# Kernel tuning notes

Hardware: AMD Instinct MI355X
Metric: run time of the kernel (lower is better)

## Reference

```python
import jax, jax.numpy as jnp
import numpy as np


def _hungarian(a):
    """Jonker-Volgenant / Kuhn-Munkres shortest-augmenting-path LAP solver.
    a: (n, n) float numpy cost matrix. Returns col_ind (int64, len n) such that
    row i is matched to column col_ind[i] (row_ind is implicitly arange(n),
    exactly like scipy.optimize.linear_sum_assignment on a square matrix).
    """
    n = a.shape[0]
    INF = np.inf
    u = np.zeros(n + 1)
    v = np.zeros(n + 1)
    p = np.zeros(n + 1, dtype=np.int64)   # p[j] = row currently matched to column j
    way = np.zeros(n + 1, dtype=np.int64)
    for i in range(1, n + 1):
        p[0] = i
        j0 = 0
        minv = np.full(n + 1, INF)
        used = np.zeros(n + 1, dtype=bool)
        while True:
            used[j0] = True
            i0 = p[j0]
            cur = a[i0 - 1] - u[i0] - v[1:]          # reduced costs of row i0
            free = ~used[1:]
            better = free & (cur < minv[1:])
            minv[1:] = np.where(better, cur, minv[1:])
            way[1:] = np.where(better, j0, way[1:])
            cand = np.where(free, minv[1:], INF)
            j1 = int(np.argmin(cand)) + 1
            delta = cand[j1 - 1]
            u[p[used]] += delta
            v[used] -= delta
            minv[1:] = np.where(free, minv[1:] - delta, minv[1:])
            j0 = j1
            if p[j0] == 0:
                break
        while j0 != 0:                               # augment along alternating path
            j1 = int(way[j0])
            p[j0] = p[j1]
            j0 = j1
    col_ind = np.zeros(n, dtype=np.int64)
    col_ind[p[1:] - 1] = np.arange(n)
    return col_ind


def _matching(input, target):
    sx = jnp.sum(input * input, axis=-1)
    sy = jnp.sum(target * target, axis=-1)
    cost = sx[:, :, None] + sy[:, None, :] - 2.0 * jnp.einsum('bkd,bmd->bkm', input, target)
    cost_np = np.asarray(jax.device_get(cost), dtype=np.float64)
    perms = np.stack([_hungarian(c) for c in cost_np])  # (B, k)
    return jnp.asarray(perms)


def setup_inputs() -> dict:
    key = jax.random.key(0)
    k1, k2 = jax.random.split(key)
    B, K, D = 512, 128, 512
    return {
        "input": jax.random.normal(k1, (B, K, D), dtype=jnp.float32),
        "target": jax.random.normal(k2, (B, K, D), dtype=jnp.float32),
    }


def reference(input, target):
    # Hungarian assignment is computed on detached costs (constant wrt grads).
    perms = _matching(input, target)                       # (B, k)
    matched_target = jnp.take_along_axis(target, perms[:, :, None], axis=1)
    # Per-batch mean over (k, d), then mean over batch == global mean (equal sizes).
    return jnp.mean((input - matched_target) ** 2)
```

## Files before the change

### kernel.cpp

```cpp
#include <hip/hip_runtime.h>
#include <hip/hip_bf16.h>

#define K_PTS 128
#define DIM   512
#define BK    32
#define XS_STRIDE 132

__device__ __forceinline__ int rdlane_i(int v, int lane) {
    return __builtin_amdgcn_readlane(v, lane);
}
__device__ __forceinline__ float rdlane_f(float v, int lane) {
    return __int_as_float(__builtin_amdgcn_readlane(__float_as_int(v), lane));
}
__device__ __forceinline__ void wave_fence() {
    asm volatile("s_waitcnt lgkmcnt(0)" ::: "memory");
}

#define DPP_ID 0xFFFFFFFFu

template <int CTRL, int RM>
__device__ __forceinline__ unsigned dpp_min1(unsigned k) {
    unsigned o = (unsigned)__builtin_amdgcn_update_dpp((int)DPP_ID, (int)k, CTRL, RM, 0xF, false);
    return min(k, o);
}
__device__ __forceinline__ unsigned wave_min_u32(unsigned k) {
    k = dpp_min1<0x111, 0xF>(k);
    k = dpp_min1<0x112, 0xF>(k);
    k = dpp_min1<0x114, 0xF>(k);
    k = dpp_min1<0x118, 0xF>(k);
    k = dpp_min1<0x142, 0xA>(k);
    k = dpp_min1<0x143, 0xC>(k);
    return (unsigned)rdlane_i((int)k, 63);
}
template <int CTRL, int RM>
__device__ __forceinline__ void dpp_min2(unsigned& best, unsigned& sec) {
    unsigned ob = (unsigned)__builtin_amdgcn_update_dpp((int)DPP_ID, (int)best, CTRL, RM, 0xF, false);
    unsigned os = (unsigned)__builtin_amdgcn_update_dpp((int)DPP_ID, (int)sec,  CTRL, RM, 0xF, false);
    sec  = min(max(best, ob), min(sec, os));
    best = min(best, ob);
}
__device__ __forceinline__ void wave_min2_u32(unsigned& best, unsigned& sec) {
    dpp_min2<0x111, 0xF>(best, sec);
    dpp_min2<0x112, 0xF>(best, sec);
    dpp_min2<0x114, 0xF>(best, sec);
    dpp_min2<0x118, 0xF>(best, sec);
    dpp_min2<0x142, 0xA>(best, sec);
    dpp_min2<0x143, 0xC>(best, sec);
    best = (unsigned)rdlane_i((int)best, 63);
    sec  = (unsigned)rdlane_i((int)sec, 63);
}

__global__ __launch_bounds__(256, 2)
void hungarian_mse_kernel(const float* __restrict__ X, const float* __restrict__ Y,
                          float* __restrict__ out, float inv_total) {
    const int b = blockIdx.x;
    const int t = threadIdx.x;

    __shared__ float A[K_PTS * K_PTS];
    __shared__ float sx_sh[K_PTS];
    __shared__ float sy_sh[K_PTS];
    __shared__ float u_sh[K_PTS];
    __shared__ int   rmatch[K_PTS];
    __shared__ int   wl[512];
    __shared__ int   wl_n;

    float* Xs = A;
    float* Ys = A + BK * XS_STRIDE;

    const float* Xg = X + (size_t)b * K_PTS * DIM;
    const float* Yg = Y + (size_t)b * K_PTS * DIM;

    float acc[8][8];
#pragma unroll
    for (int i = 0; i < 8; ++i)
#pragma unroll
        for (int j = 0; j < 8; ++j) acc[i][j] = 0.0f;

    float nrm = 0.0f;
    const int tx = t & 15;
    const int ty = t >> 4;

    for (int k0 = 0; k0 < DIM; k0 += BK) {
        __syncthreads();
#pragma unroll
        for (int i = 0; i < 4; ++i) {
            int idx = t + i * 256;
            int r  = idx >> 3;
            int kq = idx & 7;
            float4 vx = *(const float4*)(Xg + r * DIM + k0 + kq * 4);
            float4 vy = *(const float4*)(Yg + r * DIM + k0 + kq * 4);
            int kb = kq * 4;
            Xs[(kb + 0) * XS_STRIDE + r] = vx.x;
            Xs[(kb + 1) * XS_STRIDE + r] = vx.y;
            Xs[(kb + 2) * XS_STRIDE + r] = vx.z;
            Xs[(kb + 3) * XS_STRIDE + r] = vx.w;
            Ys[(kb + 0) * XS_STRIDE + r] = vy.x;
            Ys[(kb + 1) * XS_STRIDE + r] = vy.y;
            Ys[(kb + 2) * XS_STRIDE + r] = vy.z;
            Ys[(kb + 3) * XS_STRIDE + r] = vy.w;
        }
        __syncthreads();
        for (int kk = 0; kk < BK; ++kk) {
            const float* xrow = Xs + kk * XS_STRIDE;
            const float* yrow = Ys + kk * XS_STRIDE;
            float4 xa = *(const float4*)(xrow + ty * 8);
            float4 xb = *(const float4*)(xrow + ty * 8 + 4);
            float4 ya = *(const float4*)(yrow + tx * 8);
            float4 yb = *(const float4*)(yrow + tx * 8 + 4);
            float av[8] = {xa.x, xa.y, xa.z, xa.w, xb.x, xb.y, xb.z, xb.w};
            float bv[8] = {ya.x, ya.y, ya.z, ya.w, yb.x, yb.y, yb.z, yb.w};
#pragma unroll
            for (int i = 0; i < 8; ++i)
#pragma unroll
                for (int j = 0; j < 8; ++j)
                    acc[i][j] = fmaf(av[i], bv[j], acc[i][j]);
        }
        if (t < 128) {
#pragma unroll
            for (int kk = 0; kk < BK; ++kk) {
                float v = Xs[kk * XS_STRIDE + t];
                nrm = fmaf(v, v, nrm);
            }
        } else {
#pragma unroll
            for (int kk = 0; kk < BK; ++kk) {
                float v = Ys[kk * XS_STRIDE + (t - 128)];
                nrm = fmaf(v, v, nrm);
            }
        }
    }
    if (t < 128) sx_sh[t] = nrm; else sy_sh[t - 128] = nrm;
    if (t < 128) u_sh[t] = 0.0f;
    __syncthreads();
#pragma unroll
    for (int i = 0; i < 8; ++i) {
        int r = ty * 8 + i;
        float sxr = sx_sh[r];
        float4 o0, o1;
        o0.x = sxr + sy_sh[tx * 8 + 0] - 2.0f * acc[i][0];
        o0.y = sxr + sy_sh[tx * 8 + 1] - 2.0f * acc[i][1];
        o0.z = sxr + sy_sh[tx * 8 + 2] - 2.0f * acc[i][2];
        o0.w = sxr + sy_sh[tx * 8 + 3] - 2.0f * acc[i][3];
        o1.x = sxr + sy_sh[tx * 8 + 4] - 2.0f * acc[i][4];
        o1.y = sxr + sy_sh[tx * 8 + 5] - 2.0f * acc[i][5];
        o1.z = sxr + sy_sh[tx * 8 + 6] - 2.0f * acc[i][6];
        o1.w = sxr + sy_sh[tx * 8 + 7] - 2.0f * acc[i][7];
        *(float4*)&A[r * K_PTS + tx * 8]     = o0;
        *(float4*)&A[r * K_PTS + tx * 8 + 4] = o1;
    }
    __syncthreads();

    if (t < 64) {
        asm volatile("s_setprio 3");
        const int c0 = 2 * t, c1 = 2 * t + 1;
        float v0, v1;
        int p_lo = -1, p_hi = -1;

        rmatch[t] = -1; rmatch[t + 64] = -1;
        wave_fence();
        {
            float m0 = 1e30f, m1 = 1e30f;
            int a0 = 0, a1 = 0;
#pragma unroll 4
            for (int i = 0; i < K_PTS; ++i) {
                float2 cc = *(const float2*)&A[i * K_PTS + c0];
                if (cc.x < m0) { m0 = cc.x; a0 = i; }
                if (cc.y < m1) { m1 = cc.y; a1 = i; }
            }
            v0 = m0; v1 = m1;
            int w0 = atomicCAS(&rmatch[a0], -1, c0);
            if (w0 == -1) p_lo = a0;
            int w1 = atomicCAS(&rmatch[a1], -1, c1);
            if (w1 == -1) p_hi = a1;
        }
        wave_fence();

        *(float2*)&sy_sh[c0] = make_float2(v0, v1);
        wave_fence();
#pragma unroll
        for (int which = 0; which < 2; ++which) {
            int i  = t + which * 64;
            int j1 = rmatch[i];
            float mu = 1e30f;
            if (j1 >= 0) {
#pragma unroll 4
                for (int s = 0; s < 64; ++s) {
                    int jj = (s + t) & 63;
                    float2 cc = *(const float2*)&A[i * K_PTS + 2 * jj];
                    float2 vv = *(const float2*)&sy_sh[2 * jj];
                    float r0 = cc.x - vv.x;
                    float r1 = cc.y - vv.y;
                    if (2 * jj     != j1) mu = fminf(mu, r0);
                    if (2 * jj + 1 != j1) mu = fminf(mu, r1);
                }
            }
            sx_sh[i] = mu;
        }
        wave_fence();
        if (p_lo >= 0) { float mu = sx_sh[p_lo]; v0 = A[p_lo * K_PTS + c0] - mu; u_sh[p_lo] = mu; }
        if (p_hi >= 0) { float mu = sx_sh[p_hi]; v1 = A[p_hi * K_PTS + c1] - mu; u_sh[p_hi] = mu; }
        wave_fence();

        if (t == 0) {
            int n = 0;
            for (int i = 0; i < K_PTS; ++i) if (rmatch[i] < 0) wl[n++] = i;
            wl_n = n;
        }
        wave_fence();

        {
            int head = 0, tail = wl_n, steps = 0;
            int ni = -1;
            float2 nx = make_float2(0.0f, 0.0f);
            if (head < tail) {
                ni = wl[head];
                nx = *(const float2*)&A[ni * K_PTS + c0];
            }
            while (ni >= 0 && steps < 320) {
                ++steps;
                int i = ni;
                float2 cc = nx;
                int nhead = head + 1;
                int ni_spec = (nhead < tail) ? wl[nhead] : -1;

                float r0 = fmaxf(cc.x - v0, 0.0f);
                float r1 = fmaxf(cc.y - v1, 0.0f);
                unsigned k0 = (__float_as_uint(r0) & 0xFFFFFF80u) | (unsigned)c0;
                unsigned k1 = (__float_as_uint(r1) & 0xFFFFFF80u) | (unsigned)c1;
                unsigned best = min(k0, k1), sec = max(k0, k1);
                wave_min2_u32(best, sec);
                int j1 = (int)(best & 127u);
                int j2 = (int)(sec & 127u);
                float mu = __uint_as_float(best & 0xFFFFFF80u);
                float nu = __uint_as_float(sec  & 0xFFFFFF80u);
                if (t == 0) u_sh[i] = nu;
                int kO = rdlane_i((j1 & 1) ? p_hi : p_lo, j1 >> 1);
                bool strict = (mu < nu);
                if (strict && t == (j1 >> 1)) {
                    float d = nu - mu;
                    if (j1 & 1) v1 -= d; else v0 -= d;
                }
                int jA = j1;
                if (!strict && kO >= 0) {
                    int k2 = rdlane_i((j2 & 1) ? p_hi : p_lo, j2 >> 1);
                    if (k2 < 0) jA = j2;
                }
                int kOld = rdlane_i((jA & 1) ? p_hi : p_lo, jA >> 1);
                if (t == (jA >> 1)) { if (jA & 1) p_hi = i; else p_lo = i; }
                if (t == 0) {
                    rmatch[i] = jA;
                    if (kOld >= 0) { rmatch[kOld] = -1; wl[tail] = kOld; }
                }
                int tail_new = tail + ((kOld >= 0) ? 1 : 0);

                int nn;
                if (nhead < tail)          nn = ni_spec;
                else if (nhead < tail_new) nn = kOld;
                else                       nn = -1;
                if (nn >= 0) nx = *(const float2*)&A[nn * K_PTS + c0];
                ni = nn;
                head = nhead; tail = tail_new;
                wave_fence();
            }
        }

        if (t == 0) {
            int n = 0;
            for (int i = 0; i < K_PTS; ++i) if (rmatch[i] < 0) wl[n++] = i;
            wl_n = n;
        }
        wave_fence();
        const int nfree = wl_n;

        int   row_next = (nfree > 0) ? wl[0] : 0;
        float2 rc_next = make_float2(0.0f, 0.0f);
        if (nfree > 0) rc_next = *(const float2*)&A[row_next * K_PTS + c0];

        for (int idx = 0; idx < nfree; ++idx) {
            int row = row_next;
            float2 rc = rc_next;
            if (idx + 1 < nfree) {
                row_next = wl[idx + 1];
                rc_next = *(const float2*)&A[row_next * K_PTS + c0];
            }
            float u_lo_reg = u_sh[t];
            float u_hi_reg = u_sh[t + 64];
            float u_row = u_sh[row];
            float dist0 = fmaxf(rc.x - u_row - v0, 0.0f);
            float dist1 = fmaxf(rc.y - u_row - v1, 0.0f);
            int way0 = 128, way1 = 128;
            bool sc0 = false, sc1 = false;
            int j1 = 0;
            float D = 0.0f;

            while (true) {
                unsigned k0 = sc0 ? 0xFFFFFFFFu
                                  : ((__float_as_uint(dist0) & 0xFFFFFF80u) | (unsigned)c0);
                unsigned k1 = sc1 ? 0xFFFFFFFFu
                                  : ((__float_as_uint(dist1) & 0xFFFFFF80u) | (unsigned)c1);
                unsigned k = wave_min_u32(min(k0, k1));
                j1 = (int)(k & 127u);
                D  = __uint_as_float(k & 0xFFFFFF80u);
                int i1 = rdlane_i((j1 & 1) ? p_hi : p_lo, j1 >> 1);
                if (i1 < 0) break;

                if (j1 == c0) sc0 = true;
                if (j1 == c1) sc1 = true;

                float u_i1 = rdlane_f((i1 >= 64) ? u_hi_reg : u_lo_reg, i1 & 63);
                float2 aa = *(const float2*)&A[i1 * K_PTS + c0];
                float base = D - u_i1;
                if (!sc0) {
                    float cv = fmaxf((aa.x - v0) + base, 0.0f);
                    if (cv < dist0) { dist0 = cv; way0 = j1; }
                }
                if (!sc1) {
                    float cv = fmaxf((aa.y - v1) + base, 0.0f);
                    if (cv < dist1) { dist1 = cv; way1 = j1; }
                }
            }

            if (sc0) { float del = D - dist0; v0 -= del; u_sh[p_lo] += del; }
            if (sc1) { float del = D - dist1; v1 -= del; u_sh[p_hi] += del; }
            if (t == 0) u_sh[row] += D;

            int j0 = j1;
            while (true) {
                int lane0 = j0 >> 1;
                bool odd = (j0 & 1) != 0;
                int jp = rdlane_i(odd ? way1 : way0, lane0);
                int pv;
                if (jp == 128) pv = row;
                else           pv = rdlane_i((jp & 1) ? p_hi : p_lo, jp >> 1);
                if (!odd && lane0 == t) p_lo = pv;
                if ( odd && lane0 == t) p_hi = pv;
                if (jp == 128) break;
                j0 = jp;
            }
            wave_fence();
        }

        float tsum = A[p_lo * K_PTS + c0] + A[p_hi * K_PTS + c1];
#pragma unroll
        for (int m = 1; m <= 32; m <<= 1)
            tsum += __shfl_xor(tsum, m, 64);
        if (t == 0) atomicAdd(out, tsum * inv_total);
    }
}

extern "C" void kernel_launch(void* const* d_in, const int* in_sizes, int n_in,
                              void* d_out, int out_size, void* d_ws, size_t ws_size,
                              hipStream_t stream) {
    const float* X = (const float*)d_in[0];
    const float* Y = (const float*)d_in[1];
    float* out = (float*)d_out;

    const int total = in_sizes[0];
    const int B = total / (K_PTS * DIM);
    const float inv_total = 1.0f / (float)total;

    hipMemsetAsync(out, 0, out_size * sizeof(float), stream);
    hungarian_mse_kernel<<<dim3(B), dim3(256), 0, stream>>>(X, Y, out, inv_total);
}
```

Baseline: 688.3 us.

## Speculatively prefetch next Dijkstra row in shortest-augmenting-path loop

In the per-free-row augmenting-path search, each iteration now also computes the runner-up column (the minimum after excluding the just-scanned column, before distances are updated) and prefetches that row's cost pair and dual value. If the next iteration's argmin matches the speculated column, the LDS load and readlane are skipped, which takes the dependent load off the critical path. This adds an extra wave-wide min reduction and a speculative load each iteration. A wave fence in the greedy phase is also moved ahead of the next-row load.

New measurement: 735.4 us. 6.8% more time.

```diff
diff --git a/kernel.cpp b/kernel.cpp
--- a/kernel.cpp
+++ b/kernel.cpp
@@ -257,10 +257,10 @@
                 if (nhead < tail)          nn = ni_spec;
                 else if (nhead < tail_new) nn = kOld;
                 else                       nn = -1;
+                wave_fence();
                 if (nn >= 0) nx = *(const float2*)&A[nn * K_PTS + c0];
                 ni = nn;
                 head = nhead; tail = tail_new;
-                wave_fence();
             }
         }
 
@@ -293,31 +293,67 @@
             int j1 = 0;
             float D = 0.0f;
 
+            int    j_spec = -1, i_spec = -1;
+            float  u_spec = 0.0f;
+            float2 bb = make_float2(0.0f, 0.0f);
+
+            unsigned k;
+            {
+                unsigned k0 = (__float_as_uint(dist0) & 0xFFFFFF80u) | (unsigned)c0;
+                unsigned k1 = (__float_as_uint(dist1) & 0xFFFFFF80u) | (unsigned)c1;
+                k = wave_min_u32(min(k0, k1));
+            }
+
             while (true) {
+                j1 = (int)(k & 127u);
+                D  = __uint_as_float(k & 0xFFFFFF80u);
+                bool hit = (j1 == j_spec);
+                int i1 = hit ? i_spec : rdlane_i((j1 & 1) ? p_hi : p_lo, j1 >> 1);
+                if (i1 < 0) break;
+
+                if (j1 == c0) sc0 = true;
+                if (j1 == c1) sc1 = true;
+
+                float2 aa; float u_i1;
+                if (hit) {
+                    aa = bb; u_i1 = u_spec;
+                } else {
+                    aa   = *(const float2*)&A[i1 * K_PTS + c0];
+                    u_i1 = rdlane_f((i1 >= 64) ? u_hi_reg : u_lo_reg, i1 & 63);
+                }
+
+                {
+                    unsigned s0 = sc0 ? 0xFFFFFFFFu
+                                      : ((__float_as_uint(dist0) & 0xFFFFFF80u) | (unsigned)c0);
+                    unsigned s1 = sc1 ? 0xFFFFFFFFu
+                                      : ((__float_as_uint(dist1) & 0xFFFFFF80u) | (unsigned)c1);
+                    unsigned ko = wave_min_u32(min(s0, s1));
+                    int js  = (int)(ko & 127u);
+                    int is_ = rdlane_i((js & 1) ? p_hi : p_lo, js >> 1);
+                    if (is_ >= 0) {
+                        bb     = *(const float2*)&A[is_ * K_PTS + c0];
+                        u_spec = rdlane_f((is_ >= 64) ? u_hi_reg : u_lo_reg, is_ & 63);
+                        i_spec = is_; j_spec = js;
+                    } else {
+                        j_spec = -1;
+                    }
+                }
+
+                float base = D - u_i1;
+                if (!sc0) {
+                    float cv = fmaxf((aa.x - v0) + base, 0.0f);
+                    if (cv < dist0) { dist0 = cv; way0 = j1; }
+                }
+                if (!sc1) {
+                    float cv = fmaxf((aa.y - v1) + base, 0.0f);
+                    if (cv < dist1) { dist1 = cv; way1 = j1; }
+                }
+
                 unsigned k0 = sc0 ? 0xFFFFFFFFu
                                   : ((__float_as_uint(dist0) & 0xFFFFFF80u) | (unsigned)c0);
                 unsigned k1 = sc1 ? 0xFFFFFFFFu
                                   : ((__float_as_uint(dist1) & 0xFFFFFF80u) | (unsigned)c1);
-                unsigned k = wave_min_u32(min(k0, k1));
-                j1 = (int)(k & 127u);
-                D  = __uint_as_float(k & 0xFFFFFF80u);
-                int i1 = rdlane_i((j1 & 1) ? p_hi : p_lo, j1 >> 1);
-                if (i1 < 0) break;
-
-                if (j1 == c0) sc0 = true;
-                if (j1 == c1) sc1 = true;
-
-                float u_i1 = rdlane_f((i1 >= 64) ? u_hi_reg : u_lo_reg, i1 & 63);
-                float2 aa = *(const float2*)&A[i1 * K_PTS + c0];
-                float base = D - u_i1;
-                if (!sc0) {
-                    float cv = fmaxf((aa.x - v0) + base, 0.0f);
-                    if (cv < dist0) { dist0 = cv; way0 = j1; }
-                }
-                if (!sc1) {
-                    float cv = fmaxf((aa.y - v1) + base, 0.0f);
-                    if (cv < dist1) { dist1 = cv; way1 = j1; }
-                }
+                k = wave_min_u32(min(k0, k1));
             }
 
             if (sc0) { float del = D - dist0; v0 -= del; u_sh[p_lo] += del; }
```
